# Optimization experiments

Hardware: AMD Instinct MI355X
Metric: run time of the kernel (lower is better)

Reference implementation:

```python
import jax, jax.numpy as jnp
import numpy as np

D_MODEL = 768
N_HEADS = 12
HEAD_DIM = D_MODEL // N_HEADS
BATCH = 1
SEQ = 4096


def setup_inputs() -> dict:
    key = jax.random.key(0)
    ks = jax.random.split(key, 5)
    std = 1.0 / np.sqrt(D_MODEL)
    return {
        "x": jax.random.normal(ks[0], (BATCH, SEQ, D_MODEL), dtype=jnp.float32),
        "Wq": jax.random.normal(ks[1], (D_MODEL, D_MODEL), dtype=jnp.float32) * std,
        "Wk": jax.random.normal(ks[2], (D_MODEL, D_MODEL), dtype=jnp.float32) * std,
        "Wv": jax.random.normal(ks[3], (D_MODEL, D_MODEL), dtype=jnp.float32) * std,
        "Wp": jax.random.normal(ks[4], (D_MODEL, D_MODEL), dtype=jnp.float32) * std,
    }


def reference(x, Wq, Wk, Wv, Wp):
    B, S, D = x.shape
    scale = HEAD_DIM ** -0.5
    # torch Linear: y = x @ W.T ; reshape to [B, H, S, hd]
    def split_heads(y):
        return y.reshape(B, S, N_HEADS, HEAD_DIM).transpose(0, 2, 1, 3)
    q = split_heads(x @ Wq.T)
    k = split_heads(x @ Wk.T)
    v = split_heads(x @ Wv.T)
    # full [B, H, S, S] scores, as in the original module
    att = jnp.einsum("bhqd,bhkd->bhqk", q, k) * scale
    causal = jnp.tril(jnp.ones((S, S), dtype=bool))
    att = jnp.where(causal[None, None], att, -jnp.inf)
    att = jax.nn.softmax(att, axis=-1)
    y = jnp.einsum("bhqk,bhkd->bhqd", att, v)
    y = y.transpose(0, 2, 1, 3).reshape(B, S, D)
    return y @ Wp.T
```

## Files before the change

### kernel.cpp

```cpp
#include <hip/hip_runtime.h>
#include <hip/hip_bf16.h>
#include <stdint.h>

#define DM 768
#define SQ 4096
#define NH 12

typedef __bf16 bf16;
typedef __bf16 bf16x8 __attribute__((ext_vector_type(8)));
typedef float floatx4 __attribute__((ext_vector_type(4)));
typedef short short4v __attribute__((ext_vector_type(4)));

#if defined(__has_builtin)
#if __has_builtin(__builtin_amdgcn_mfma_f32_16x16x16bf16_1k)
#define HAVE_MFMA16 1
#endif
#endif
#ifndef HAVE_MFMA16
#define HAVE_MFMA16 0
#endif

typedef __attribute__((address_space(1))) const uint32_t cu32_g;
typedef __attribute__((address_space(3))) uint32_t u32_l;

__device__ __forceinline__ uint16_t f2bf(float f) {
  uint32_t u = __builtin_bit_cast(uint32_t, f);
  u += 0x7fff + ((u >> 16) & 1);
  return (uint16_t)(u >> 16);
}

__device__ __forceinline__ uint32_t pk2(float lo, float hi) {
  __hip_bfloat162 h = __float22bfloat162_rn(float2{lo, hi});
  uint32_t u;
  __builtin_memcpy(&u, &h, 4);
  return u;
}

__device__ __forceinline__ float bflo(uint32_t u) {
  return __builtin_bit_cast(float, u << 16);
}
__device__ __forceinline__ float bfhi(uint32_t u) {
  return __builtin_bit_cast(float, u & 0xffff0000u);
}

__device__ __forceinline__ void async16(const bf16* g, bf16* l) {
  __builtin_amdgcn_global_load_lds((cu32_g*)g, (u32_l*)l, 16, 0, 0);
}

struct MapT { uint16_t v[160]; };
static constexpr MapT make_map() {
  MapT m{};
  int idx = 0;
  for (int nit = 16; nit >= 1; --nit)
    for (int qb = 63; qb >= 0; --qb) {
      int len = (qb + 1) * 64;
      int nch = (len + 1023) >> 10;
      for (int c = nch - 1; c >= 0; --c) {
        int cs = c * 1024;
        int ce = (len < cs + 1024) ? len : cs + 1024;
        int ni = (ce - cs) >> 6;
        if (ni == nit) m.v[idx++] = (uint16_t)(qb * 4 + c);
      }
    }
  return m;
}
__device__ __constant__ MapT kMap = make_map();

__global__ __launch_bounds__(256) void cvt_kernel(
    const float* __restrict__ x, const float* __restrict__ wq,
    const float* __restrict__ wk, const float* __restrict__ wv,
    const float* __restrict__ wp, bf16* __restrict__ xb, bf16* __restrict__ wqb,
    bf16* __restrict__ wkb, bf16* __restrict__ wvb, bf16* __restrict__ wpb) {
  const int XQ = (SQ * DM) / 4;
  const int WQ = (DM * DM) / 4;
  int t = blockIdx.x * 256 + threadIdx.x;
  const float* src;
  bf16* dst;
  int local;
  if (t < XQ) { src = x;  dst = xb;  local = t; }
  else if (t < XQ + WQ)     { src = wq; dst = wqb; local = t - XQ; }
  else if (t < XQ + 2 * WQ) { src = wk; dst = wkb; local = t - XQ - WQ; }
  else if (t < XQ + 3 * WQ) { src = wv; dst = wvb; local = t - XQ - 2 * WQ; }
  else                      { src = wp; dst = wpb; local = t - XQ - 3 * WQ; }
  float4 v = ((const float4*)src)[local];
  ushort4 o;
  o.x = f2bf(v.x); o.y = f2bf(v.y); o.z = f2bf(v.z); o.w = f2bf(v.w);
  ((ushort4*)dst)[local] = o;
}

__device__ __forceinline__ void gemm_core(const bf16* __restrict__ A,
                                          const bf16* __restrict__ B, int m0,
                                          int n0, floatx4 (&acc)[4][4]) {
  __shared__ bf16 lA[2 * 4096];
  __shared__ bf16 lB[2 * 4096];
  const int tid = threadIdx.x;
  const int lane = tid & 63;
  const int w = tid >> 6;

  const int r0 = w * 32 + (lane >> 2);
  const int ke = (((lane & 3) ^ ((lane >> 3) & 3))) * 8;
  const bf16* gA0 = A + (size_t)(m0 + r0) * DM + ke;
  const bf16* gA1 = A + (size_t)(m0 + r0 + 16) * DM + ke;
  const bf16* gB0 = B + (size_t)(n0 + r0) * DM + ke;
  const bf16* gB1 = B + (size_t)(n0 + r0 + 16) * DM + ke;

  async16(gA0, lA + w * 1024); async16(gA1, lA + w * 1024 + 512);
  async16(gB0, lB + w * 1024); async16(gB1, lB + w * 1024 + 512);
  gA0 += 32; gA1 += 32; gB0 += 32; gB1 += 32;

  const int mrow = (w >> 1) * 64 + (lane & 15);
  const int nrow = (w & 1) * 64 + (lane & 15);
  const int cswz = ((lane >> 4) ^ ((lane >> 1) & 3)) * 8;

  for (int kt = 0; kt < DM / 32; ++kt) {
    __syncthreads();
    if (kt + 1 < DM / 32) {
      const int nb = ((kt + 1) & 1) * 4096;
      async16(gA0, lA + nb + w * 1024); async16(gA1, lA + nb + w * 1024 + 512);
      async16(gB0, lB + nb + w * 1024); async16(gB1, lB + nb + w * 1024 + 512);
      gA0 += 32; gA1 += 32; gB0 += 32; gB1 += 32;
    }
    const int cb = (kt & 1) * 4096;
    bf16x8 a[4], b[4];
#pragma unroll
    for (int mt = 0; mt < 4; ++mt)
      a[mt] = *(const bf16x8*)&lA[cb + (mrow + mt * 16) * 32 + cswz];
#pragma unroll
    for (int nt = 0; nt < 4; ++nt)
      b[nt] = *(const bf16x8*)&lB[cb + (nrow + nt * 16) * 32 + cswz];
#pragma unroll
    for (int mt = 0; mt < 4; ++mt)
#pragma unroll
      for (int nt = 0; nt < 4; ++nt)
        acc[mt][nt] = __builtin_amdgcn_mfma_f32_16x16x32_bf16(
            a[mt], b[nt], acc[mt][nt], 0, 0, 0);
  }
}

__global__ __launch_bounds__(256) void qkv_kernel(
    const bf16* __restrict__ xb, const bf16* __restrict__ wq,
    const bf16* __restrict__ wk, const bf16* __restrict__ wv,
    bf16* __restrict__ Qb, bf16* __restrict__ Kb, bf16* __restrict__ Vtb) {
  const int z = blockIdx.z;
  const bf16* B = (z == 0) ? wq : (z == 1) ? wk : wv;
  const int m0 = blockIdx.x * 128, n0 = blockIdx.y * 128;
  floatx4 acc[4][4] = {};
  gemm_core(xb, B, m0, n0, acc);
  const int lane = threadIdx.x & 63, w = threadIdx.x >> 6;
  const int quad = lane >> 4, ql = lane & 15;
  const float qs = (z == 0) ? 0.18033688011112042f : 1.0f;
  if (z < 2) {
    bf16* C = (z == 0) ? Qb : Kb;
#pragma unroll
    for (int mt = 0; mt < 4; ++mt)
#pragma unroll
      for (int nt = 0; nt < 4; ++nt) {
        int row = m0 + (w >> 1) * 64 + mt * 16 + quad * 4;
        int col = n0 + (w & 1) * 64 + nt * 16 + ql;
#pragma unroll
        for (int r = 0; r < 4; ++r)
          *(uint16_t*)&C[(size_t)(row + r) * DM + col] = f2bf(acc[mt][nt][r] * qs);
      }
  } else {
#pragma unroll
    for (int mt = 0; mt < 4; ++mt)
#pragma unroll
      for (int nt = 0; nt < 4; ++nt) {
        int row = m0 + (w >> 1) * 64 + mt * 16 + quad * 4;
        int col = n0 + (w & 1) * 64 + nt * 16 + ql;
        uint32_t lo = pk2(acc[mt][nt][0], acc[mt][nt][1]);
        uint32_t hi = pk2(acc[mt][nt][2], acc[mt][nt][3]);
        *(uint2*)&Vtb[(size_t)col * SQ + row] = make_uint2(lo, hi);
      }
  }
}

__global__ __launch_bounds__(256) void proj_kernel(
    const bf16* __restrict__ Ob, const bf16* __restrict__ wp,
    float* __restrict__ out) {
  __shared__ bf16 lA[2 * 2048];
  __shared__ bf16 lB[2 * 4096];
  const int tid = threadIdx.x, lane = tid & 63, w = tid >> 6;
  const int m0 = blockIdx.x * 64, n0 = blockIdx.y * 128;

  const int ke = (((lane & 3) ^ ((lane >> 3) & 3))) * 8;
  const bf16* gA = Ob + (size_t)(m0 + w * 16 + (lane >> 2)) * DM + ke;
  const bf16* gB0 = wp + (size_t)(n0 + w * 32 + (lane >> 2)) * DM + ke;
  const bf16* gB1 = wp + (size_t)(n0 + w * 32 + (lane >> 2) + 16) * DM + ke;

  async16(gA, lA + w * 512);
  async16(gB0, lB + w * 1024); async16(gB1, lB + w * 1024 + 512);
  gA += 32; gB0 += 32; gB1 += 32;

  const int mrow = (w >> 1) * 32 + (lane & 15);
  const int nrow = (w & 1) * 64 + (lane & 15);
  const int cswz = ((lane >> 4) ^ ((lane >> 1) & 3)) * 8;
  floatx4 acc[2][4] = {};

  for (int kt = 0; kt < DM / 32; ++kt) {
    __syncthreads();
    if (kt + 1 < DM / 32) {
      const int nbA = ((kt + 1) & 1) * 2048, nbB = ((kt + 1) & 1) * 4096;
      async16(gA, lA + nbA + w * 512);
      async16(gB0, lB + nbB + w * 1024); async16(gB1, lB + nbB + w * 1024 + 512);
      gA += 32; gB0 += 32; gB1 += 32;
    }
    const int cbA = (kt & 1) * 2048, cbB = (kt & 1) * 4096;
    bf16x8 a[2], b[4];
#pragma unroll
    for (int mt = 0; mt < 2; ++mt)
      a[mt] = *(const bf16x8*)&lA[cbA + (mrow + mt * 16) * 32 + cswz];
#pragma unroll
    for (int nt = 0; nt < 4; ++nt)
      b[nt] = *(const bf16x8*)&lB[cbB + (nrow + nt * 16) * 32 + cswz];
#pragma unroll
    for (int mt = 0; mt < 2; ++mt)
#pragma unroll
      for (int nt = 0; nt < 4; ++nt)
        acc[mt][nt] = __builtin_amdgcn_mfma_f32_16x16x32_bf16(
            a[mt], b[nt], acc[mt][nt], 0, 0, 0);
  }
  const int quad = lane >> 4, ql = lane & 15;
#pragma unroll
  for (int mt = 0; mt < 2; ++mt)
#pragma unroll
    for (int nt = 0; nt < 4; ++nt) {
      int row = m0 + (w >> 1) * 32 + mt * 16 + quad * 4;
      int col = n0 + (w & 1) * 64 + nt * 16 + ql;
#pragma unroll
      for (int r = 0; r < 4; ++r)
        out[(size_t)(row + r) * DM + col] = acc[mt][nt][r];
    }
}

__global__ __launch_bounds__(256, 5) void attn_kernel(
    const bf16* __restrict__ Qb, const bf16* __restrict__ Kb,
    const bf16* __restrict__ Vtb, uint16_t* __restrict__ OpartB,
    float* __restrict__ Lpart, bf16* __restrict__ Ob) {
#if HAVE_MFMA16
  __shared__ __align__(16) char smem[32768];
#else
  __shared__ __align__(16) char smem[40960];
  bf16* lPt = (bf16*)(smem + 32768);
#endif
  const int tid = threadIdx.x, lane = tid & 63, w = tid >> 6;
  const int quad = lane >> 4, ql = lane & 15;
  const int qh = w & 1;
  const int kh = w >> 1;

  int b = blockIdx.x;
  int h = b % NH;
  int i = b / NH;
  int e = kMap.v[i];
  int qb = e >> 2, c = e & 3;
  const int kv0 = c * 1024;
  const int qlen = (qb + 1) * 64;
  const int kv_end = min(qlen, kv0 + 1024);
  const int n_it = (kv_end - kv0) >> 6;
  const bool diag = (kv_end == qlen);

  bf16x8 qf[2][2];
#pragma unroll
  for (int nt = 0; nt < 2; ++nt)
#pragma unroll
    for (int kt = 0; kt < 2; ++kt)
      qf[nt][kt] = *(const bf16x8*)&Qb[(size_t)(qb * 64 + qh * 32 + nt * 16 + ql) * DM +
                                       h * 64 + kt * 32 + quad * 8];

  const int src_e = (((lane & 3) ^ ((lane >> 3) & 3))) * 8;
  const bf16* gK[2];
  const bf16* gV[2];
#pragma unroll
  for (int t = 0; t < 2; ++t) {
    int o = t * 4096 + w * 1024 + lane * 16;
    int cK = o >> 12, rK = (o & 4095) >> 6;
    gK[t] = Kb + (size_t)(kv0 + rK) * DM + h * 64 + cK * 32 + src_e;
    int dV = w * 16 + (lane >> 2);
    gV[t] = Vtb + (size_t)(h * 64 + dV) * SQ + kv0 + t * 32 + src_e;
  }

#pragma unroll
  for (int t = 0; t < 2; ++t) {
    async16(gK[t], (bf16*)(smem + t * 4096 + w * 1024));
    async16(gV[t], (bf16*)(smem + 8192 + t * 4096 + w * 1024));
    gK[t] += 64 * DM;
    gV[t] += 64;
  }

  floatx4 o_acc[4][2] = {};
  float l_s[2] = {0.f, 0.f};
  const int cswz = ((lane >> 4) ^ ((lane >> 1) & 3)) * 8;

  for (int j = 0; j < n_it; ++j) {
    __syncthreads();
    if (j + 1 < n_it) {
      char* dst = smem + ((j + 1) & 1) * 16384;
#pragma unroll
      for (int t = 0; t < 2; ++t) {
        async16(gK[t], (bf16*)(dst + t * 4096 + w * 1024));
        async16(gV[t], (bf16*)(dst + 8192 + t * 4096 + w * 1024));
        gK[t] += 64 * DM;
        gV[t] += 64;
      }
    }
    const char* cbuf = smem + (j & 1) * 16384;
    const bf16* kbuf = (const bf16*)cbuf;
    const char* vbuf = cbuf + 8192;

    floatx4 s[2][2] = {};
    __builtin_amdgcn_s_setprio(1);
#pragma unroll
    for (int kt = 0; kt < 2; ++kt)
#pragma unroll
      for (int mt = 0; mt < 2; ++mt) {
        bf16x8 a = *(const bf16x8*)&kbuf[kt * 2048 + (kh * 32 + mt * 16 + ql) * 32 + cswz];
#pragma unroll
        for (int nt = 0; nt < 2; ++nt)
          s[mt][nt] = __builtin_amdgcn_mfma_f32_16x16x32_bf16(a, qf[nt][kt],
                                                              s[mt][nt], 0, 0, 0);
      }
    __builtin_amdgcn_s_setprio(0);

    if (diag && j == n_it - 1) {
#pragma unroll
      for (int mt = 0; mt < 2; ++mt)
#pragma unroll
        for (int nt = 0; nt < 2; ++nt) {
          const int qpos = qh * 32 + nt * 16 + ql;
#pragma unroll
          for (int r = 0; r < 4; ++r) {
            int kpos = kh * 32 + mt * 16 + quad * 4 + r;
            if (kpos > qpos) s[mt][nt][r] = -1e30f;
          }
        }
    }

    uint2 pp[2][2];
#pragma unroll
    for (int nt = 0; nt < 2; ++nt) {
      float tsum[2];
#pragma unroll
      for (int mt = 0; mt < 2; ++mt) {
        float p0 = __builtin_amdgcn_exp2f(s[mt][nt][0]);
        float p1 = __builtin_amdgcn_exp2f(s[mt][nt][1]);
        float p2 = __builtin_amdgcn_exp2f(s[mt][nt][2]);
        float p3 = __builtin_amdgcn_exp2f(s[mt][nt][3]);
        pp[mt][nt] = make_uint2(pk2(p0, p1), pk2(p2, p3));
        tsum[mt] = (p0 + p1) + (p2 + p3);
      }
      l_s[nt] += tsum[0] + tsum[1];
    }

#if HAVE_MFMA16
    __builtin_amdgcn_s_setprio(1);
#pragma unroll
    for (int mt = 0; mt < 2; ++mt) {
      short4v bfr[2];
#pragma unroll
      for (int nt = 0; nt < 2; ++nt) {
        union { uint2 u; short4v v; } pb;
        pb.u = pp[mt][nt];
        bfr[nt] = pb.v;
      }
      const char* vbase = vbuf + kh * 4096 +
          (((mt * 2 + (quad >> 1)) ^ ((ql >> 1) & 3)) * 16) +
          (quad & 1) * 8;
#pragma unroll
      for (int mtd = 0; mtd < 4; ++mtd) {
        short4v a = *(const short4v*)(vbase + (mtd * 16 + ql) * 64);
#pragma unroll
        for (int nt = 0; nt < 2; ++nt)
          o_acc[mtd][nt] = __builtin_amdgcn_mfma_f32_16x16x16bf16_1k(
              a, bfr[nt], o_acc[mtd][nt], 0, 0, 0);
      }
    }
    __builtin_amdgcn_s_setprio(0);
#else
    bf16* lp = lPt + w * 1024;
    {
#pragma unroll
      for (int nt = 0; nt < 2; ++nt) {
        int q32 = nt * 16 + ql;
        int key = (q32 >> 1) & 7;
#pragma unroll
        for (int mtp = 0; mtp < 2; ++mtp) {
          int slot = mtp * 4 + quad;
          *(uint2*)((char*)lp + q32 * 64 + ((slot ^ key) * 8)) = pp[mtp][nt];
        }
      }
      bf16x8 bp[2];
#pragma unroll
      for (int nt = 0; nt < 2; ++nt) {
        int q32 = nt * 16 + ql;
        int key = (q32 >> 1) & 7;
        union { uint2 u[2]; bf16x8 v; } pb;
        pb.u[0] = *(uint2*)((char*)lp + q32 * 64 + (((2 * quad) ^ key) * 8));
        pb.u[1] = *(uint2*)((char*)lp + q32 * 64 + (((2 * quad + 1) ^ key) * 8));
        bp[nt] = pb.v;
      }
      __builtin_amdgcn_s_setprio(1);
#pragma unroll
      for (int mtd = 0; mtd < 4; ++mtd) {
        bf16x8 a = *(const bf16x8*)((const bf16*)vbuf + kh * 2048 +
                                    (mtd * 16 + ql) * 32 + cswz);
#pragma unroll
        for (int nt = 0; nt < 2; ++nt)
          o_acc[mtd][nt] = __builtin_amdgcn_mfma_f32_16x16x32_bf16(
              a, bp[nt], o_acc[mtd][nt], 0, 0, 0);
      }
      __builtin_amdgcn_s_setprio(0);
    }
#endif
  }

  char* fb = smem + ((n_it & 1) * 16384);
  char* lb = smem + (((n_it - 1) & 1) * 16384);
  __syncthreads();
  if (kh == 1) {
    char* po = fb + (w - 2) * 8192;
#pragma unroll
    for (int nt = 0; nt < 2; ++nt)
#pragma unroll
      for (int mtd = 0; mtd < 4; ++mtd)
        *(floatx4*)(po + (nt * 4 + mtd) * 1024 + lane * 16) = o_acc[mtd][nt];
    float2* pl = (float2*)(lb + (w - 2) * 512);
    pl[lane] = make_float2(l_s[0], l_s[1]);
  }
  __syncthreads();
  if (kh == 0) {
    char* po = fb + w * 8192;
#pragma unroll
    for (int nt = 0; nt < 2; ++nt)
#pragma unroll
      for (int mtd = 0; mtd < 4; ++mtd)
        o_acc[mtd][nt] += *(const floatx4*)(po + (nt * 4 + mtd) * 1024 + lane * 16);
    float2 l2 = ((const float2*)(lb + w * 512))[lane];
    l_s[0] += l2.x;
    l_s[1] += l2.y;

    float lf[2];
#pragma unroll
    for (int nt = 0; nt < 2; ++nt) {
      float ls = l_s[nt];
      ls += __shfl_xor(ls, 16);
      ls += __shfl_xor(ls, 32);
      lf[nt] = ls;
    }

    if (qb < 16) {
#pragma unroll
      for (int nt = 0; nt < 2; ++nt) {
        float rl = 1.0f / lf[nt];
        int qg = qb * 64 + qh * 32 + nt * 16 + ql;
#pragma unroll
        for (int mtd = 0; mtd < 4; ++mtd) {
          uint32_t lo = pk2(o_acc[mtd][nt][0] * rl, o_acc[mtd][nt][1] * rl);
          uint32_t hi = pk2(o_acc[mtd][nt][2] * rl, o_acc[mtd][nt][3] * rl);
          *(uint2*)&Ob[(size_t)qg * DM + h * 64 + mtd * 16 + quad * 4] =
              make_uint2(lo, hi);
        }
      }
    } else {
      const int ps = (h * 64 + qb) * 4 + c;
#pragma unroll
      for (int nt = 0; nt < 2; ++nt) {
        int q = qh * 32 + nt * 16 + ql;
        if (quad == 0) Lpart[ps * 64 + q] = lf[nt];
#pragma unroll
        for (int mtd = 0; mtd < 4; ++mtd) {
          uint32_t lo = pk2(o_acc[mtd][nt][0], o_acc[mtd][nt][1]);
          uint32_t hi = pk2(o_acc[mtd][nt][2], o_acc[mtd][nt][3]);
          *(uint2*)&OpartB[(size_t)ps * 4096 + q * 64 + mtd * 16 + quad * 4] =
              make_uint2(lo, hi);
        }
      }
    }
  }
}

__global__ __launch_bounds__(256) void combine_kernel(
    const uint16_t* __restrict__ OpartB, const float* __restrict__ Lpart,
    bf16* __restrict__ Ob) {
  int b = blockIdx.x;
  int h = b % NH, qb = 16 + b / NH;
  int nch = (qb + 16) >> 4;
  int t = threadIdx.x;
  int q = t >> 2, dh = (t & 3) * 16;
  int ps0 = (h * 64 + qb) * 4;

  float acc[16] = {};
  float L = 0.f;
#pragma unroll
  for (int cc = 0; cc < 4; ++cc)
    if (cc < nch) {
      L += Lpart[(ps0 + cc) * 64 + q];
      const uint4* p =
          (const uint4*)(OpartB + (size_t)(ps0 + cc) * 4096 + q * 64 + dh);
#pragma unroll
      for (int g = 0; g < 2; ++g) {
        uint4 u = p[g];
        acc[g * 8 + 0] += bflo(u.x); acc[g * 8 + 1] += bfhi(u.x);
        acc[g * 8 + 2] += bflo(u.y); acc[g * 8 + 3] += bfhi(u.y);
        acc[g * 8 + 4] += bflo(u.z); acc[g * 8 + 5] += bfhi(u.z);
        acc[g * 8 + 6] += bflo(u.w); acc[g * 8 + 7] += bfhi(u.w);
      }
    }
  float rl = 1.0f / L;
  bf16* dst = &Ob[(size_t)(qb * 64 + q) * DM + h * 64 + dh];
#pragma unroll
  for (int g = 0; g < 2; ++g) {
    uint4 u;
    u.x = pk2(acc[g * 8 + 0] * rl, acc[g * 8 + 1] * rl);
    u.y = pk2(acc[g * 8 + 2] * rl, acc[g * 8 + 3] * rl);
    u.z = pk2(acc[g * 8 + 4] * rl, acc[g * 8 + 5] * rl);
    u.w = pk2(acc[g * 8 + 6] * rl, acc[g * 8 + 7] * rl);
    *(uint4*)&dst[g * 8] = u;
  }
}

extern "C" void kernel_launch(void* const* d_in, const int* in_sizes, int n_in,
                              void* d_out, int out_size, void* d_ws,
                              size_t ws_size, hipStream_t stream) {
  const float* x  = (const float*)d_in[0];
  const float* wq = (const float*)d_in[1];
  const float* wk = (const float*)d_in[2];
  const float* wv = (const float*)d_in[3];
  const float* wp = (const float*)d_in[4];
  char* ws = (char*)d_ws;
  float* Lpart = (float*)(ws);
  bf16* xb   = (bf16*)(ws);
  bf16* wqb  = (bf16*)(ws + 6291456);
  bf16* wkb  = (bf16*)(ws + 7471104);
  bf16* wvb  = (bf16*)(ws + 8650752);
  bf16* wpb  = (bf16*)(ws + 9830400);
  bf16* Qb   = (bf16*)(ws + 11010048);
  bf16* Kb   = (bf16*)(ws + 17301504);
  bf16* Vtb  = (bf16*)(ws + 23592960);
  bf16* Ob   = (bf16*)(ws + 29884416);
  uint16_t* OpartB = (uint16_t*)(ws + 36175872);

  cvt_kernel<<<5376, 256, 0, stream>>>(x, wq, wk, wv, wp, xb, wqb, wkb, wvb, wpb);
  qkv_kernel<<<dim3(32, 6, 3), 256, 0, stream>>>(xb, wqb, wkb, wvb, Qb, Kb, Vtb);
  attn_kernel<<<1920, 256, 0, stream>>>(Qb, Kb, Vtb, OpartB, Lpart, Ob);
  combine_kernel<<<576, 256, 0, stream>>>(OpartB, Lpart, Ob);
  proj_kernel<<<dim3(64, 6), 256, 0, stream>>>(Ob, wpb, (float*)d_out);
}
```

Measured before the change: 163.4 us.

## Make attention kernel persistent with cost-balanced static work ranges per block

Replaces the one-work-item-per-block launch of 1920 attention blocks with 1280 blocks. Each block loops over a contiguous range of (head, query-block, KV-chunk) units taken from a compile-time table that balances the total KV iterations evenly across blocks. The goal is to reduce tail imbalance and per-block launch overhead. In exchange, each block runs its units serially and has extra syncs between units, and ranges are split by cumulative cost rather than by any hardware-aware measure.

Result: slower. 241.2 us (+47.6%).

```diff
diff --git a/kernel.cpp b/kernel.cpp
--- a/kernel.cpp
+++ b/kernel.cpp
@@ -47,9 +47,10 @@
   __builtin_amdgcn_global_load_lds((cu32_g*)g, (u32_l*)l, 16, 0, 0);
 }
 
-struct MapT { uint16_t v[160]; };
-static constexpr MapT make_map() {
-  MapT m{};
+struct SchedT { uint16_t unit[160]; uint16_t start[1281]; };
+static constexpr SchedT make_sched() {
+  SchedT s{};
+  int cost[160] = {};
   int idx = 0;
   for (int nit = 16; nit >= 1; --nit)
     for (int qb = 63; qb >= 0; --qb) {
@@ -59,12 +60,26 @@
         int cs = c * 1024;
         int ce = (len < cs + 1024) ? len : cs + 1024;
         int ni = (ce - cs) >> 6;
-        if (ni == nit) m.v[idx++] = (uint16_t)(qb * 4 + c);
-      }
-    }
-  return m;
-}
-__device__ __constant__ MapT kMap = make_map();
+        if (ni == nit) { s.unit[idx] = (uint16_t)(qb * 4 + c); cost[idx] = ni; ++idx; }
+      }
+    }
+  long total = 0;
+  for (int i = 0; i < 160; ++i) total += cost[i];
+  total *= 12;
+  long acc = 0;
+  int b = 0;
+  s.start[0] = 0;
+  for (int g = 0; g < 1920; ++g) {
+    acc += cost[g / 12];
+    while (b + 1 < 1280 && acc * 1280 >= (long)(b + 1) * total) {
+      ++b;
+      s.start[b] = (uint16_t)(g + 1);
+    }
+  }
+  for (int bb = b + 1; bb <= 1280; ++bb) s.start[bb] = 1920;
+  return s;
+}
+__device__ __constant__ SchedT kSched = make_sched();
 
 __global__ __launch_bounds__(256) void cvt_kernel(
     const float* __restrict__ x, const float* __restrict__ wq,
@@ -247,231 +262,234 @@
   const int quad = lane >> 4, ql = lane & 15;
   const int qh = w & 1;
   const int kh = w >> 1;
-
-  int b = blockIdx.x;
-  int h = b % NH;
-  int i = b / NH;
-  int e = kMap.v[i];
-  int qb = e >> 2, c = e & 3;
-  const int kv0 = c * 1024;
-  const int qlen = (qb + 1) * 64;
-  const int kv_end = min(qlen, kv0 + 1024);
-  const int n_it = (kv_end - kv0) >> 6;
-  const bool diag = (kv_end == qlen);
-
-  bf16x8 qf[2][2];
-#pragma unroll
-  for (int nt = 0; nt < 2; ++nt)
-#pragma unroll
-    for (int kt = 0; kt < 2; ++kt)
-      qf[nt][kt] = *(const bf16x8*)&Qb[(size_t)(qb * 64 + qh * 32 + nt * 16 + ql) * DM +
-                                       h * 64 + kt * 32 + quad * 8];
-
   const int src_e = (((lane & 3) ^ ((lane >> 3) & 3))) * 8;
-  const bf16* gK[2];
-  const bf16* gV[2];
-#pragma unroll
-  for (int t = 0; t < 2; ++t) {
-    int o = t * 4096 + w * 1024 + lane * 16;
-    int cK = o >> 12, rK = (o & 4095) >> 6;
-    gK[t] = Kb + (size_t)(kv0 + rK) * DM + h * 64 + cK * 32 + src_e;
-    int dV = w * 16 + (lane >> 2);
-    gV[t] = Vtb + (size_t)(h * 64 + dV) * SQ + kv0 + t * 32 + src_e;
-  }
-
-#pragma unroll
-  for (int t = 0; t < 2; ++t) {
-    async16(gK[t], (bf16*)(smem + t * 4096 + w * 1024));
-    async16(gV[t], (bf16*)(smem + 8192 + t * 4096 + w * 1024));
-    gK[t] += 64 * DM;
-    gV[t] += 64;
-  }
-
-  floatx4 o_acc[4][2] = {};
-  float l_s[2] = {0.f, 0.f};
   const int cswz = ((lane >> 4) ^ ((lane >> 1) & 3)) * 8;
 
-  for (int j = 0; j < n_it; ++j) {
+  const int g0 = kSched.start[blockIdx.x];
+  const int g1 = kSched.start[blockIdx.x + 1];
+
+  for (int g = g0; g < g1; ++g) {
+    const int i = g / 12;
+    const int h = g - i * 12;
+    const int e = kSched.unit[i];
+    const int qb = e >> 2, c = e & 3;
+    const int kv0 = c * 1024;
+    const int qlen = (qb + 1) * 64;
+    const int kv_end = min(qlen, kv0 + 1024);
+    const int n_it = (kv_end - kv0) >> 6;
+    const bool diag = (kv_end == qlen);
+
+    bf16x8 qf[2][2];
+#pragma unroll
+    for (int nt = 0; nt < 2; ++nt)
+#pragma unroll
+      for (int kt = 0; kt < 2; ++kt)
+        qf[nt][kt] = *(const bf16x8*)&Qb[(size_t)(qb * 64 + qh * 32 + nt * 16 + ql) * DM +
+                                         h * 64 + kt * 32 + quad * 8];
+
+    const bf16* gK[2];
+    const bf16* gV[2];
+#pragma unroll
+    for (int t = 0; t < 2; ++t) {
+      int o = t * 4096 + w * 1024 + lane * 16;
+      int cK = o >> 12, rK = (o & 4095) >> 6;
+      gK[t] = Kb + (size_t)(kv0 + rK) * DM + h * 64 + cK * 32 + src_e;
+      int dV = w * 16 + (lane >> 2);
+      gV[t] = Vtb + (size_t)(h * 64 + dV) * SQ + kv0 + t * 32 + src_e;
+    }
+
     __syncthreads();
-    if (j + 1 < n_it) {
-      char* dst = smem + ((j + 1) & 1) * 16384;
-#pragma unroll
-      for (int t = 0; t < 2; ++t) {
-        async16(gK[t], (bf16*)(dst + t * 4096 + w * 1024));
-        async16(gV[t], (bf16*)(dst + 8192 + t * 4096 + w * 1024));
-        gK[t] += 64 * DM;
-        gV[t] += 64;
-      }
-    }
-    const char* cbuf = smem + (j & 1) * 16384;
-    const bf16* kbuf = (const bf16*)cbuf;
-    const char* vbuf = cbuf + 8192;
-
-    floatx4 s[2][2] = {};
-    __builtin_amdgcn_s_setprio(1);
-#pragma unroll
-    for (int kt = 0; kt < 2; ++kt)
+#pragma unroll
+    for (int t = 0; t < 2; ++t) {
+      async16(gK[t], (bf16*)(smem + t * 4096 + w * 1024));
+      async16(gV[t], (bf16*)(smem + 8192 + t * 4096 + w * 1024));
+      gK[t] += 64 * DM;
+      gV[t] += 64;
+    }
+
+    floatx4 o_acc[4][2] = {};
+    float l_s[2] = {0.f, 0.f};
+
+    for (int j = 0; j < n_it; ++j) {
+      __syncthreads();
+      if (j + 1 < n_it) {
+        char* dst = smem + ((j + 1) & 1) * 16384;
+#pragma unroll
+        for (int t = 0; t < 2; ++t) {
+          async16(gK[t], (bf16*)(dst + t * 4096 + w * 1024));
+          async16(gV[t], (bf16*)(dst + 8192 + t * 4096 + w * 1024));
+          gK[t] += 64 * DM;
+          gV[t] += 64;
+        }
+      }
+      const char* cbuf = smem + (j & 1) * 16384;
+      const bf16* kbuf = (const bf16*)cbuf;
+      const char* vbuf = cbuf + 8192;
+
+      floatx4 s[2][2] = {};
+      __builtin_amdgcn_s_setprio(1);
+#pragma unroll
+      for (int kt = 0; kt < 2; ++kt)
+#pragma unroll
+        for (int mt = 0; mt < 2; ++mt) {
+          bf16x8 a = *(const bf16x8*)&kbuf[kt * 2048 + (kh * 32 + mt * 16 + ql) * 32 + cswz];
+#pragma unroll
+          for (int nt = 0; nt < 2; ++nt)
+            s[mt][nt] = __builtin_amdgcn_mfma_f32_16x16x32_bf16(a, qf[nt][kt],
+                                                                s[mt][nt], 0, 0, 0);
+        }
+      __builtin_amdgcn_s_setprio(0);
+
+      if (diag && j == n_it - 1) {
+#pragma unroll
+        for (int mt = 0; mt < 2; ++mt)
+#pragma unroll
+          for (int nt = 0; nt < 2; ++nt) {
+            const int qpos = qh * 32 + nt * 16 + ql;
+#pragma unroll
+            for (int r = 0; r < 4; ++r) {
+              int kpos = kh * 32 + mt * 16 + quad * 4 + r;
+              if (kpos > qpos) s[mt][nt][r] = -1e30f;
+            }
+          }
+      }
+
+      uint2 pp[2][2];
+#pragma unroll
+      for (int nt = 0; nt < 2; ++nt) {
+        float tsum[2];
+#pragma unroll
+        for (int mt = 0; mt < 2; ++mt) {
+          float p0 = __builtin_amdgcn_exp2f(s[mt][nt][0]);
+          float p1 = __builtin_amdgcn_exp2f(s[mt][nt][1]);
+          float p2 = __builtin_amdgcn_exp2f(s[mt][nt][2]);
+          float p3 = __builtin_amdgcn_exp2f(s[mt][nt][3]);
+          pp[mt][nt] = make_uint2(pk2(p0, p1), pk2(p2, p3));
+          tsum[mt] = (p0 + p1) + (p2 + p3);
+        }
+        l_s[nt] += tsum[0] + tsum[1];
+      }
+
+#if HAVE_MFMA16
+      __builtin_amdgcn_s_setprio(1);
 #pragma unroll
       for (int mt = 0; mt < 2; ++mt) {
-        bf16x8 a = *(const bf16x8*)&kbuf[kt * 2048 + (kh * 32 + mt * 16 + ql) * 32 + cswz];
-#pragma unroll
-        for (int nt = 0; nt < 2; ++nt)
-          s[mt][nt] = __builtin_amdgcn_mfma_f32_16x16x32_bf16(a, qf[nt][kt],
-                                                              s[mt][nt], 0, 0, 0);
-      }
-    __builtin_amdgcn_s_setprio(0);
-
-    if (diag && j == n_it - 1) {
-#pragma unroll
-      for (int mt = 0; mt < 2; ++mt)
+        short4v bfr[2];
 #pragma unroll
         for (int nt = 0; nt < 2; ++nt) {
-          const int qpos = qh * 32 + nt * 16 + ql;
-#pragma unroll
-          for (int r = 0; r < 4; ++r) {
-            int kpos = kh * 32 + mt * 16 + quad * 4 + r;
-            if (kpos > qpos) s[mt][nt][r] = -1e30f;
+          union { uint2 u; short4v v; } pb;
+          pb.u = pp[mt][nt];
+          bfr[nt] = pb.v;
+        }
+        const char* vbase = vbuf + kh * 4096 +
+            (((mt * 2 + (quad >> 1)) ^ ((ql >> 1) & 3)) * 16) +
+            (quad & 1) * 8;
+#pragma unroll
+        for (int mtd = 0; mtd < 4; ++mtd) {
+          short4v a = *(const short4v*)(vbase + (mtd * 16 + ql) * 64);
+#pragma unroll
+          for (int nt = 0; nt < 2; ++nt)
+            o_acc[mtd][nt] = __builtin_amdgcn_mfma_f32_16x16x16bf16_1k(
+                a, bfr[nt], o_acc[mtd][nt], 0, 0, 0);
+        }
+      }
+      __builtin_amdgcn_s_setprio(0);
+#else
+      bf16* lp = lPt + w * 1024;
+      {
+#pragma unroll
+        for (int nt = 0; nt < 2; ++nt) {
+          int q32 = nt * 16 + ql;
+          int key = (q32 >> 1) & 7;
+#pragma unroll
+          for (int mtp = 0; mtp < 2; ++mtp) {
+            int slot = mtp * 4 + quad;
+            *(uint2*)((char*)lp + q32 * 64 + ((slot ^ key) * 8)) = pp[mtp][nt];
           }
         }
-    }
-
-    uint2 pp[2][2];
-#pragma unroll
-    for (int nt = 0; nt < 2; ++nt) {
-      float tsum[2];
-#pragma unroll
-      for (int mt = 0; mt < 2; ++mt) {
-        float p0 = __builtin_amdgcn_exp2f(s[mt][nt][0]);
-        float p1 = __builtin_amdgcn_exp2f(s[mt][nt][1]);
-        float p2 = __builtin_amdgcn_exp2f(s[mt][nt][2]);
-        float p3 = __builtin_amdgcn_exp2f(s[mt][nt][3]);
-        pp[mt][nt] = make_uint2(pk2(p0, p1), pk2(p2, p3));
-        tsum[mt] = (p0 + p1) + (p2 + p3);
-      }
-      l_s[nt] += tsum[0] + tsum[1];
-    }
-
-#if HAVE_MFMA16
-    __builtin_amdgcn_s_setprio(1);
-#pragma unroll
-    for (int mt = 0; mt < 2; ++mt) {
-      short4v bfr[2];
+        bf16x8 bp[2];
+#pragma unroll
+        for (int nt = 0; nt < 2; ++nt) {
+          int q32 = nt * 16 + ql;
+          int key = (q32 >> 1) & 7;
+          union { uint2 u[2]; bf16x8 v; } pb;
+          pb.u[0] = *(uint2*)((char*)lp + q32 * 64 + (((2 * quad) ^ key) * 8));
+          pb.u[1] = *(uint2*)((char*)lp + q32 * 64 + (((2 * quad + 1) ^ key) * 8));
+          bp[nt] = pb.v;
+        }
+#pragma unroll
+        for (int mtd = 0; mtd < 4; ++mtd) {
+          bf16x8 a = *(const bf16x8*)((const bf16*)vbuf + kh * 2048 +
+                                      (mtd * 16 + ql) * 32 + cswz);
+#pragma unroll
+          for (int nt = 0; nt < 2; ++nt)
+            o_acc[mtd][nt] = __builtin_amdgcn_mfma_f32_16x16x32_bf16(
+                a, bp[nt], o_acc[mtd][nt], 0, 0, 0);
+        }
+      }
+#endif
+    }
+
+    char* fb = smem + ((n_it & 1) * 16384);
+    char* lb = smem + (((n_it - 1) & 1) * 16384);
+    __syncthreads();
+    if (kh == 1) {
+      char* po = fb + (w - 2) * 8192;
+#pragma unroll
+      for (int nt = 0; nt < 2; ++nt)
+#pragma unroll
+        for (int mtd = 0; mtd < 4; ++mtd)
+          *(floatx4*)(po + (nt * 4 + mtd) * 1024 + lane * 16) = o_acc[mtd][nt];
+      float2* pl = (float2*)(lb + (w - 2) * 512);
+      pl[lane] = make_float2(l_s[0], l_s[1]);
+    }
+    __syncthreads();
+    if (kh == 0) {
+      char* po = fb + w * 8192;
+#pragma unroll
+      for (int nt = 0; nt < 2; ++nt)
+#pragma unroll
+        for (int mtd = 0; mtd < 4; ++mtd)
+          o_acc[mtd][nt] += *(const floatx4*)(po + (nt * 4 + mtd) * 1024 + lane * 16);
+      float2 l2 = ((const float2*)(lb + w * 512))[lane];
+      l_s[0] += l2.x;
+      l_s[1] += l2.y;
+
+      float lf[2];
 #pragma unroll
       for (int nt = 0; nt < 2; ++nt) {
-        union { uint2 u; short4v v; } pb;
-        pb.u = pp[mt][nt];
-        bfr[nt] = pb.v;
-      }
-      const char* vbase = vbuf + kh * 4096 +
-          (((mt * 2 + (quad >> 1)) ^ ((ql >> 1) & 3)) * 16) +
-          (quad & 1) * 8;
-#pragma unroll
-      for (int mtd = 0; mtd < 4; ++mtd) {
-        short4v a = *(const short4v*)(vbase + (mtd * 16 + ql) * 64);
-#pragma unroll
-        for (int nt = 0; nt < 2; ++nt)
-          o_acc[mtd][nt] = __builtin_amdgcn_mfma_f32_16x16x16bf16_1k(
-              a, bfr[nt], o_acc[mtd][nt], 0, 0, 0);
-      }
-    }
-    __builtin_amdgcn_s_setprio(0);
-#else
-    bf16* lp = lPt + w * 1024;
-    {
-#pragma unroll
-      for (int nt = 0; nt < 2; ++nt) {
-        int q32 = nt * 16 + ql;
-        int key = (q32 >> 1) & 7;
-#pragma unroll
-        for (int mtp = 0; mtp < 2; ++mtp) {
-          int slot = mtp * 4 + quad;
-          *(uint2*)((char*)lp + q32 * 64 + ((slot ^ key) * 8)) = pp[mtp][nt];
-        }
-      }
-      bf16x8 bp[2];
-#pragma unroll
-      for (int nt = 0; nt < 2; ++nt) {
-        int q32 = nt * 16 + ql;
-        int key = (q32 >> 1) & 7;
-        union { uint2 u[2]; bf16x8 v; } pb;
-        pb.u[0] = *(uint2*)((char*)lp + q32 * 64 + (((2 * quad) ^ key) * 8));
-        pb.u[1] = *(uint2*)((char*)lp + q32 * 64 + (((2 * quad + 1) ^ key) * 8));
-        bp[nt] = pb.v;
-      }
-      __builtin_amdgcn_s_setprio(1);
-#pragma unroll
-      for (int mtd = 0; mtd < 4; ++mtd) {
-        bf16x8 a = *(const bf16x8*)((const bf16*)vbuf + kh * 2048 +
-                                    (mtd * 16 + ql) * 32 + cswz);
-#pragma unroll
-        for (int nt = 0; nt < 2; ++nt)
-          o_acc[mtd][nt] = __builtin_amdgcn_mfma_f32_16x16x32_bf16(
-              a, bp[nt], o_acc[mtd][nt], 0, 0, 0);
-      }
-      __builtin_amdgcn_s_setprio(0);
-    }
-#endif
-  }
-
-  char* fb = smem + ((n_it & 1) * 16384);
-  char* lb = smem + (((n_it - 1) & 1) * 16384);
-  __syncthreads();
-  if (kh == 1) {
-    char* po = fb + (w - 2) * 8192;
-#pragma unroll
-    for (int nt = 0; nt < 2; ++nt)
-#pragma unroll
-      for (int mtd = 0; mtd < 4; ++mtd)
-        *(floatx4*)(po + (nt * 4 + mtd) * 1024 + lane * 16) = o_acc[mtd][nt];
-    float2* pl = (float2*)(lb + (w - 2) * 512);
-    pl[lane] = make_float2(l_s[0], l_s[1]);
-  }
-  __syncthreads();
-  if (kh == 0) {
-    char* po = fb + w * 8192;
-#pragma unroll
-    for (int nt = 0; nt < 2; ++nt)
-#pragma unroll
-      for (int mtd = 0; mtd < 4; ++mtd)
-        o_acc[mtd][nt] += *(const floatx4*)(po + (nt * 4 + mtd) * 1024 + lane * 16);
-    float2 l2 = ((const float2*)(lb + w * 512))[lane];
-    l_s[0] += l2.x;
-    l_s[1] += l2.y;
-
-    float lf[2];
-#pragma unroll
-    for (int nt = 0; nt < 2; ++nt) {
-      float ls = l_s[nt];
-      ls += __shfl_xor(ls, 16);
-      ls += __shfl_xor(ls, 32);
-      lf[nt] = ls;
-    }
-
-    if (qb < 16) {
-#pragma unroll
-      for (int nt = 0; nt < 2; ++nt) {
-        float rl = 1.0f / lf[nt];
-        int qg = qb * 64 + qh * 32 + nt * 16 + ql;
-#pragma unroll
-        for (int mtd = 0; mtd < 4; ++mtd) {
-          uint32_t lo = pk2(o_acc[mtd][nt][0] * rl, o_acc[mtd][nt][1] * rl);
-          uint32_t hi = pk2(o_acc[mtd][nt][2] * rl, o_acc[mtd][nt][3] * rl);
-          *(uint2*)&Ob[(size_t)qg * DM + h * 64 + mtd * 16 + quad * 4] =
-              make_uint2(lo, hi);
-        }
-      }
-    } else {
-      const int ps = (h * 64 + qb) * 4 + c;
-#pragma unroll
-      for (int nt = 0; nt < 2; ++nt) {
-        int q = qh * 32 + nt * 16 + ql;
-        if (quad == 0) Lpart[ps * 64 + q] = lf[nt];
-#pragma unroll
-        for (int mtd = 0; mtd < 4; ++mtd) {
-          uint32_t lo = pk2(o_acc[mtd][nt][0], o_acc[mtd][nt][1]);
-          uint32_t hi = pk2(o_acc[mtd][nt][2], o_acc[mtd][nt][3]);
-          *(uint2*)&OpartB[(size_t)ps * 4096 + q * 64 + mtd * 16 + quad * 4] =
-              make_uint2(lo, hi);
+        float ls = l_s[nt];
+        ls += __shfl_xor(ls, 16);
+        ls += __shfl_xor(ls, 32);
+        lf[nt] = ls;
+      }
+
+      if (qb < 16) {
+#pragma unroll
+        for (int nt = 0; nt < 2; ++nt) {
+          float rl = 1.0f / lf[nt];
+          int qg = qb * 64 + qh * 32 + nt * 16 + ql;
+#pragma unroll
+          for (int mtd = 0; mtd < 4; ++mtd) {
+            uint32_t lo = pk2(o_acc[mtd][nt][0] * rl, o_acc[mtd][nt][1] * rl);
+            uint32_t hi = pk2(o_acc[mtd][nt][2] * rl, o_acc[mtd][nt][3] * rl);
+            *(uint2*)&Ob[(size_t)qg * DM + h * 64 + mtd * 16 + quad * 4] =
+                make_uint2(lo, hi);
+          }
+        }
+      } else {
+        const int ps = (h * 64 + qb) * 4 + c;
+#pragma unroll
+        for (int nt = 0; nt < 2; ++nt) {
+          int q = qh * 32 + nt * 16 + ql;
+          if (quad == 0) Lpart[ps * 64 + q] = lf[nt];
+#pragma unroll
+          for (int mtd = 0; mtd < 4; ++mtd) {
+            uint32_t lo = pk2(o_acc[mtd][nt][0], o_acc[mtd][nt][1]);
+            uint32_t hi = pk2(o_acc[mtd][nt][2], o_acc[mtd][nt][3]);
+            *(uint2*)&OpartB[(size_t)ps * 4096 + q * 64 + mtd * 16 + quad * 4] =
+                make_uint2(lo, hi);
+          }
         }
       }
     }
@@ -541,7 +559,7 @@
 
   cvt_kernel<<<5376, 256, 0, stream>>>(x, wq, wk, wv, wp, xb, wqb, wkb, wvb, wpb);
   qkv_kernel<<<dim3(32, 6, 3), 256, 0, stream>>>(xb, wqb, wkb, wvb, Qb, Kb, Vtb);
-  attn_kernel<<<1920, 256, 0, stream>>>(Qb, Kb, Vtb, OpartB, Lpart, Ob);
+  attn_kernel<<<1280, 256, 0, stream>>>(Qb, Kb, Vtb, OpartB, Lpart, Ob);
   combine_kernel<<<576, 256, 0, stream>>>(OpartB, Lpart, Ob);
   proj_kernel<<<dim3(64, 6), 256, 0, stream>>>(Ob, wpb, (float*)d_out);
 }
```
